# Optimization experiments

Hardware: AMD Instinct MI355X
Metric: run time of the kernel (lower is better)

The kernel has to match this reference:

```python
import jax, jax.numpy as jnp
import numpy as np

DIM = 128  # feature dim, used for 1/sqrt(dim) scaling


def setup_inputs() -> dict:
    key = jax.random.key(0)
    kq, kk, kv, kpq, kpk = jax.random.split(key, 5)
    B, S, D = 16, 2048, DIM
    return {
        "Q": jax.random.normal(kq, (B, S, D), dtype=jnp.float32),
        "K": jax.random.normal(kk, (B, S, D), dtype=jnp.float32),
        "V": jax.random.normal(kv, (B, S, D), dtype=jnp.float32),
        "p_q": jax.random.uniform(kpq, (B, S, 1), dtype=jnp.float32),
        "p_k": jax.random.uniform(kpk, (B, S, 1), dtype=jnp.float32),
    }


def reference(Q, K, V, p_q, p_k):
    # A: [B, Sq, Sk] scaled dot-product scores
    scale = 1.0 / jnp.sqrt(jnp.asarray(DIM, dtype=Q.dtype))
    A = jnp.einsum("bqd,bkd->bqk", Q, K) * scale
    # multiplicative pre-gate: p_q [B,Sq,1] * p_k^T [B,1,Sk]
    A = A * p_q * jnp.swapaxes(p_k, -2, -1)
    W = jax.nn.softmax(A, axis=-1)
    return jnp.einsum("bqk,bkd->bqd", W, V)
```

## Files before the change

kernel.cpp:

```cpp
#include <hip/hip_runtime.h>
#include <hip/hip_fp16.h>


typedef _Float16 f16x8 __attribute__((ext_vector_type(8)));
typedef float f32x16 __attribute__((ext_vector_type(16)));
typedef unsigned int u32x4 __attribute__((ext_vector_type(4)));

#define S_LEN 2048
#define DD 128
#define TILE_BYTES 16384
#define NT 32

#define EXP2(x) __builtin_amdgcn_exp2f(x)

__device__ __forceinline__ unsigned int pk2(float a, float b) {
  __half2 h = __float22half2_rn(make_float2(a, b));
  return __builtin_bit_cast(unsigned int, h);
}

__device__ __forceinline__ void st8(void* dst, const float v[8]) {
  u32x4 u;
  u[0] = pk2(v[0], v[1]);
  u[1] = pk2(v[2], v[3]);
  u[2] = pk2(v[4], v[5]);
  u[3] = pk2(v[6], v[7]);
  *(u32x4*)dst = u;
}

__device__ __forceinline__ void gld16(const void* g, void* l) {
  __builtin_amdgcn_global_load_lds(
      (const __attribute__((address_space(1))) unsigned int*)g,
      (__attribute__((address_space(3))) unsigned int*)l, 16, 0, 0);
}

__global__ __launch_bounds__(256) void prep_q_k(const float* __restrict__ Q,
                                                const float* __restrict__ pq,
                                                char* __restrict__ qh) {
  size_t i = ((size_t)blockIdx.x * 256 + threadIdx.x) * 8;
  const float g = pq[i >> 7] * 0.12751743343158394f;
  float4 a = *(const float4*)(Q + i);
  float4 b = *(const float4*)(Q + i + 4);
  float v[8] = {a.x * g, a.y * g, a.z * g, a.w * g,
                b.x * g, b.y * g, b.z * g, b.w * g};
  st8(qh + i * 2, v);
}

__global__ __launch_bounds__(256) void prep_kv(
    const float* __restrict__ K, const float* __restrict__ V,
    const float* __restrict__ pk, char* __restrict__ kimg,
    char* __restrict__ vimg) {
  __shared__ float vt[64 * 132];
  const int t = threadIdx.x;
  const int bid = blockIdx.x;
  const int bq = bid & 15;
  const int kt = bid >> 4;
  const size_t rowbase = (size_t)bq * S_LEN + kt * 64;

#pragma unroll
  for (int cc = 0; cc < 8; ++cc) {
    const int f = cc * 256 + t;
    const int row = f >> 5;
    const int col = (f & 31) * 4;
    *(float4*)(vt + row * 132 + col) = *(const float4*)(V + (rowbase + row) * DD + col);
  }

  char* kdst = kimg + (size_t)(bq * NT + kt) * TILE_BYTES;
#pragma unroll
  for (int cc = 0; cc < 4; ++cc) {
    const int p0 = (cc * 256 + t) * 16;
    const int key = p0 >> 8;
    const int d0 = ((p0 & 255) ^ ((key & 7) << 4)) >> 1;
    const float g = pk[rowbase + key];
    const float* src = K + (rowbase + key) * DD + d0;
    float4 a = *(const float4*)(src);
    float4 b = *(const float4*)(src + 4);
    float v[8] = {a.x * g, a.y * g, a.z * g, a.w * g,
                  b.x * g, b.y * g, b.z * g, b.w * g};
    st8(kdst + p0, v);
  }

  __syncthreads();

  char* vdst = vimg + (size_t)(bq * NT + kt) * TILE_BYTES;
#pragma unroll
  for (int cc = 0; cc < 4; ++cc) {
    const int p0 = (cc * 256 + t) * 16;
    const int dcol = p0 >> 7;
    const int key0 = ((p0 & 127) ^ ((dcol & 7) << 4)) >> 1;
    float v[8];
#pragma unroll
    for (int j = 0; j < 8; ++j) v[j] = vt[(key0 + j) * 132 + dcol];
    st8(vdst + p0, v);
  }
}

__global__ __launch_bounds__(512, 2) void attn_main(const char* __restrict__ qh,
                                                    const char* __restrict__ kimg,
                                                    const char* __restrict__ vimg,
                                                    float* __restrict__ out) {
  __shared__ float4 ldsraw[4352];
  char* lds = (char*)ldsraw;
  const int tid = threadIdx.x;
  const int wid = tid >> 6;
  const int qs = wid >> 1;
  const int ks = wid & 1;
  const int lane = tid & 63;
  const int c = lane & 31;
  const int h = lane >> 5;
  const int swz = (c & 7) << 4;
  const int bid = blockIdx.x;
  const int bq = 2 * (bid & 7) + ((bid >> 3) & 1);
  const int qt = bid >> 4;
  const int q0 = qt * 128 + qs * 32;

  f16x8 qf[8];
  const char* qrow = qh + (size_t)(bq * S_LEN + q0 + c) * (DD * 2);
#pragma unroll
  for (int kc = 0; kc < 8; ++kc) qf[kc] = *(const f16x8*)(qrow + kc * 32 + h * 16);

  f32x16 acc[4];
#pragma unroll
  for (int d = 0; d < 4; ++d) {
#pragma unroll
    for (int r = 0; r < 16; ++r) acc[d][r] = 0.f;
  }
  float m_run = -1.0e30f, l_run = 0.f;

  const char* kb = kimg + (size_t)bq * (NT * TILE_BYTES);
  const char* vb = vimg + (size_t)bq * (NT * TILE_BYTES);

#pragma unroll
  for (int j = 0; j < 2; ++j) {
    gld16(kb + j * 8192 + tid * 16, lds + j * 8192 + tid * 16);
    gld16(vb + j * 8192 + tid * 16, lds + TILE_BYTES + j * 8192 + tid * 16);
  }

  for (int kt = 0; kt < NT; ++kt) {
    __syncthreads();
    const int cur = (kt & 1) << 15;
    if (kt + 1 < NT) {
      const int nxt = ((kt + 1) & 1) << 15;
      const char* kn = kb + (size_t)(kt + 1) * TILE_BYTES;
      const char* vn = vb + (size_t)(kt + 1) * TILE_BYTES;
#pragma unroll
      for (int j = 0; j < 2; ++j) {
        gld16(kn + j * 8192 + tid * 16, lds + nxt + j * 8192 + tid * 16);
        gld16(vn + j * 8192 + tid * 16, lds + nxt + TILE_BYTES + j * 8192 + tid * 16);
      }
    }
    const char* kl = lds + cur;
    const char* vl = lds + cur + TILE_BYTES;

    f32x16 s;
#pragma unroll
    for (int r = 0; r < 16; ++r) s[r] = 0.f;
    __builtin_amdgcn_s_setprio(1);
#pragma unroll
    for (int kc = 0; kc < 8; ++kc) {
      f16x8 kf = *(const f16x8*)(kl + (ks * 32 + c) * 256 + ((kc * 32 + h * 16) ^ swz));
      s = __builtin_amdgcn_mfma_f32_32x32x16_f16(kf, qf[kc], s, 0, 0, 0);
    }
    __builtin_amdgcn_s_setprio(0);

    float cm = s[0];
#pragma unroll
    for (int r = 1; r < 16; ++r) cm = fmaxf(cm, s[r]);
    cm = fmaxf(cm, __shfl_xor(cm, 32));
    if (__any(cm > m_run + 11.0f)) {
      const float mn = fmaxf(m_run, cm);
      const float al = EXP2(m_run - mn);
      m_run = mn;
      l_run *= al;
#pragma unroll
      for (int d = 0; d < 4; ++d) {
#pragma unroll
        for (int r = 0; r < 16; ++r) acc[d][r] *= al;
      }
    }
    float ps = 0.f;
#pragma unroll
    for (int r = 0; r < 16; ++r) {
      s[r] = EXP2(s[r] - m_run);
      ps += s[r];
    }
    l_run += ps;

#pragma unroll
    for (int kc = 0; kc < 2; ++kc) {
      const int A = kc * 8;
      const int Bb = A + 4;
      unsigned pA0 = pk2(s[A + 0], s[A + 1]);
      unsigned pA1 = pk2(s[A + 2], s[A + 3]);
      unsigned pB0 = pk2(s[Bb + 0], s[Bb + 1]);
      unsigned pB1 = pk2(s[Bb + 2], s[Bb + 3]);
      unsigned own0 = h ? pB0 : pA0;
      unsigned own1 = h ? pB1 : pA1;
      unsigned snd0 = h ? pA0 : pB0;
      unsigned snd1 = h ? pA1 : pB1;
      unsigned rcv0 = __shfl_xor(snd0, 32);
      unsigned rcv1 = __shfl_xor(snd1, 32);
      u32x4 pw;
      pw[0] = h ? rcv0 : own0;
      pw[1] = h ? rcv1 : own1;
      pw[2] = h ? own0 : rcv0;
      pw[3] = h ? own1 : rcv1;
      f16x8 pf = __builtin_bit_cast(f16x8, pw);
      const int kci = ks * 2 + kc;
      __builtin_amdgcn_s_setprio(1);
#pragma unroll
      for (int d = 0; d < 4; ++d) {
        f16x8 vf = *(const f16x8*)(vl + (d * 32 + c) * 128 + ((kci * 32 + h * 16) ^ swz));
        acc[d] = __builtin_amdgcn_mfma_f32_32x32x16_f16(vf, pf, acc[d], 0, 0, 0);
      }
      __builtin_amdgcn_s_setprio(0);
    }
  }

  l_run += __shfl_xor(l_run, 32);

  __syncthreads();
  float2* ml = (float2*)(lds + 65536);
  if (h == 0) ml[wid * 32 + c] = make_float2(m_run, l_run);
  __syncthreads();
  const float2 po = ml[(wid ^ 1) * 32 + c];
  const float ms = fmaxf(m_run, po.x);
  const float lstar = l_run * EXP2(m_run - ms) + po.y * EXP2(po.x - ms);
  const float w = EXP2(m_run - ms) / lstar;

  char* T = lds;
  if (ks == 0) {
#pragma unroll
    for (int d = 0; d < 4; ++d) {
#pragma unroll
      for (int rr = 0; rr < 4; ++rr) {
        const int dd = d * 32 + rr * 8 + h * 4;
        float4 v4;
        v4.x = acc[d][rr * 4 + 0] * w;
        v4.y = acc[d][rr * 4 + 1] * w;
        v4.z = acc[d][rr * 4 + 2] * w;
        v4.w = acc[d][rr * 4 + 3] * w;
        *(float4*)(T + (qs * 32 + c) * 512 + ((dd * 4) ^ swz)) = v4;
      }
    }
  }
  __syncthreads();
  if (ks == 1) {
#pragma unroll
    for (int d = 0; d < 4; ++d) {
#pragma unroll
      for (int rr = 0; rr < 4; ++rr) {
        const int dd = d * 32 + rr * 8 + h * 4;
        float4* p = (float4*)(T + (qs * 32 + c) * 512 + ((dd * 4) ^ swz));
        float4 t = *p;
        t.x += acc[d][rr * 4 + 0] * w;
        t.y += acc[d][rr * 4 + 1] * w;
        t.z += acc[d][rr * 4 + 2] * w;
        t.w += acc[d][rr * 4 + 3] * w;
        *p = t;
      }
    }
  }
  __syncthreads();

  float* obase = out + ((size_t)bq * S_LEN + qt * 128) * DD;
#pragma unroll
  for (int p = 0; p < 8; ++p) {
    const int idx = p * 512 + tid;
    const int q = idx >> 5;
    const int d0 = (idx & 31) * 4;
    float4 v4 = *(const float4*)(T + q * 512 + ((d0 * 4) ^ ((q & 7) << 4)));
    *(float4*)(obase + q * DD + d0) = v4;
  }
}

extern "C" void kernel_launch(void* const* d_in, const int* in_sizes, int n_in,
                              void* d_out, int out_size, void* d_ws, size_t ws_size,
                              hipStream_t stream) {
  const float* Q = (const float*)d_in[0];
  const float* K = (const float*)d_in[1];
  const float* V = (const float*)d_in[2];
  const float* pq = (const float*)d_in[3];
  const float* pk = (const float*)d_in[4];
  float* out = (float*)d_out;
  char* ws = (char*)d_ws;
  char* qh = ws;
  char* kimg = ws + (8u << 20);
  char* vimg = ws + (16u << 20);

  prep_q_k<<<2048, 256, 0, stream>>>(Q, pq, qh);
  prep_kv<<<512, 256, 0, stream>>>(K, V, pk, kimg, vimg);
  attn_main<<<256, 512, 0, stream>>>(qh, kimg, vimg, out);
}
```

Before: 66.33 us.

## Split attention over two key halves and merge partials in separate kernel

Splits the key/value sequence into two halves so attn_main launches 512 blocks instead of 256, each processing 16 key tiles. Every block writes an fp16 partial output plus its running max and sum, and a new merge2 kernel combines the two halves with softmax rescaling into the fp32 output. This targets low occupancy on a GPU with many CUs (256 blocks underfill it), at the cost of an extra launch, extra global traffic for the partials, and fp16 rounding of intermediate outputs. It also tree-reduces the max and splits the exp-sum into two accumulators to shorten dependency chains, and changes launch bounds to 4 blocks per SM with a smaller LDS array.

```diff
diff --git a/kernel.cpp b/kernel.cpp
--- a/kernel.cpp
+++ b/kernel.cpp
@@ -10,6 +10,9 @@
 #define DD 128
 #define TILE_BYTES 16384
 #define NT 32
+#define NTH 16
+#define PART_ROWS 32768
+#define PART_STRIDE 4194304
 
 #define EXP2(x) __builtin_amdgcn_exp2f(x)
 
@@ -94,11 +97,12 @@
   }
 }
 
-__global__ __launch_bounds__(512, 2) void attn_main(const char* __restrict__ qh,
+__global__ __launch_bounds__(512, 4) void attn_main(const char* __restrict__ qh,
                                                     const char* __restrict__ kimg,
                                                     const char* __restrict__ vimg,
-                                                    float* __restrict__ out) {
-  __shared__ float4 ldsraw[4352];
+                                                    _Float16* __restrict__ part,
+                                                    float2* __restrict__ mlws) {
+  __shared__ float4 ldsraw[4224];
   char* lds = (char*)ldsraw;
   const int tid = threadIdx.x;
   const int wid = tid >> 6;
@@ -110,7 +114,8 @@
   const int swz = (c & 7) << 4;
   const int bid = blockIdx.x;
   const int bq = 2 * (bid & 7) + ((bid >> 3) & 1);
-  const int qt = bid >> 4;
+  const int qt = (bid >> 4) & 15;
+  const int kh = bid >> 8;
   const int q0 = qt * 128 + qs * 32;
 
   f16x8 qf[8];
@@ -126,8 +131,8 @@
   }
   float m_run = -1.0e30f, l_run = 0.f;
 
-  const char* kb = kimg + (size_t)bq * (NT * TILE_BYTES);
-  const char* vb = vimg + (size_t)bq * (NT * TILE_BYTES);
+  const char* kb = kimg + (size_t)(bq * NT + kh * NTH) * TILE_BYTES;
+  const char* vb = vimg + (size_t)(bq * NT + kh * NTH) * TILE_BYTES;
 
 #pragma unroll
   for (int j = 0; j < 2; ++j) {
@@ -135,10 +140,10 @@
     gld16(vb + j * 8192 + tid * 16, lds + TILE_BYTES + j * 8192 + tid * 16);
   }
 
-  for (int kt = 0; kt < NT; ++kt) {
+  for (int kt = 0; kt < NTH; ++kt) {
     __syncthreads();
     const int cur = (kt & 1) << 15;
-    if (kt + 1 < NT) {
+    if (kt + 1 < NTH) {
       const int nxt = ((kt + 1) & 1) << 15;
       const char* kn = kb + (size_t)(kt + 1) * TILE_BYTES;
       const char* vn = vb + (size_t)(kt + 1) * TILE_BYTES;
@@ -162,9 +167,12 @@
     }
     __builtin_amdgcn_s_setprio(0);
 
-    float cm = s[0];
-#pragma unroll
-    for (int r = 1; r < 16; ++r) cm = fmaxf(cm, s[r]);
+    float m0 = fmaxf(s[0], s[1]), m1 = fmaxf(s[2], s[3]);
+    float m2 = fmaxf(s[4], s[5]), m3 = fmaxf(s[6], s[7]);
+    float m4 = fmaxf(s[8], s[9]), m5 = fmaxf(s[10], s[11]);
+    float m6 = fmaxf(s[12], s[13]), m7 = fmaxf(s[14], s[15]);
+    m0 = fmaxf(m0, m1); m2 = fmaxf(m2, m3); m4 = fmaxf(m4, m5); m6 = fmaxf(m6, m7);
+    float cm = fmaxf(fmaxf(m0, m2), fmaxf(m4, m6));
     cm = fmaxf(cm, __shfl_xor(cm, 32));
     if (__any(cm > m_run + 11.0f)) {
       const float mn = fmaxf(m_run, cm);
@@ -177,13 +185,13 @@
         for (int r = 0; r < 16; ++r) acc[d][r] *= al;
       }
     }
-    float ps = 0.f;
-#pragma unroll
-    for (int r = 0; r < 16; ++r) {
-      s[r] = EXP2(s[r] - m_run);
-      ps += s[r];
-    }
-    l_run += ps;
+    float ps0 = 0.f, ps1 = 0.f;
+#pragma unroll
+    for (int r = 0; r < 8; ++r) {
+      s[r] = EXP2(s[r] - m_run);         ps0 += s[r];
+      s[r + 8] = EXP2(s[r + 8] - m_run); ps1 += s[r + 8];
+    }
+    l_run += ps0 + ps1;
 
 #pragma unroll
     for (int kc = 0; kc < 2; ++kc) {
@@ -262,15 +270,50 @@
   }
   __syncthreads();
 
-  float* obase = out + ((size_t)bq * S_LEN + qt * 128) * DD;
-#pragma unroll
-  for (int p = 0; p < 8; ++p) {
+  const size_t prow = (size_t)bq * S_LEN + qt * 128;
+  _Float16* pdst = part + (size_t)kh * PART_STRIDE + prow * 128;
+#pragma unroll
+  for (int p = 0; p < 4; ++p) {
     const int idx = p * 512 + tid;
-    const int q = idx >> 5;
-    const int d0 = (idx & 31) * 4;
-    float4 v4 = *(const float4*)(T + q * 512 + ((d0 * 4) ^ ((q & 7) << 4)));
-    *(float4*)(obase + q * DD + d0) = v4;
-  }
+    const int row = idx >> 4;
+    const int d0 = (idx & 15) * 8;
+    const int swzT = (row & 7) << 4;
+    float4 A = *(const float4*)(T + row * 512 + ((d0 * 4) ^ swzT));
+    float4 Bv = *(const float4*)(T + row * 512 + (((d0 * 4) + 16) ^ swzT));
+    float v[8] = {A.x, A.y, A.z, A.w, Bv.x, Bv.y, Bv.z, Bv.w};
+    st8((void*)(pdst + row * 128 + d0), v);
+  }
+  if (ks == 0 && h == 0)
+    mlws[(size_t)kh * PART_ROWS + prow + qs * 32 + c] = make_float2(ms, lstar);
+}
+
+__global__ __launch_bounds__(256) void merge2(const _Float16* __restrict__ part,
+                                              const float2* __restrict__ mlws,
+                                              float* __restrict__ out) {
+  const int t = blockIdx.x * 256 + threadIdx.x;
+  const int d0 = (t & 15) * 8;
+  const int r = t >> 4;
+  const float2 a = mlws[r];
+  const float2 b = mlws[PART_ROWS + r];
+  const float M = fmaxf(a.x, b.x);
+  const float wa = a.y * EXP2(a.x - M);
+  const float wb = b.y * EXP2(b.x - M);
+  const float inv = 1.f / (wa + wb);
+  const float fa = wa * inv, fb = wb * inv;
+  const f16x8 pa = *(const f16x8*)(part + (size_t)r * 128 + d0);
+  const f16x8 pb = *(const f16x8*)(part + PART_STRIDE + (size_t)r * 128 + d0);
+  float4 o0, o1;
+  o0.x = fa * (float)pa[0] + fb * (float)pb[0];
+  o0.y = fa * (float)pa[1] + fb * (float)pb[1];
+  o0.z = fa * (float)pa[2] + fb * (float)pb[2];
+  o0.w = fa * (float)pa[3] + fb * (float)pb[3];
+  o1.x = fa * (float)pa[4] + fb * (float)pb[4];
+  o1.y = fa * (float)pa[5] + fb * (float)pb[5];
+  o1.z = fa * (float)pa[6] + fb * (float)pb[6];
+  o1.w = fa * (float)pa[7] + fb * (float)pb[7];
+  float* orow = out + (size_t)r * 128 + d0;
+  *(float4*)orow = o0;
+  *(float4*)(orow + 4) = o1;
 }
 
 extern "C" void kernel_launch(void* const* d_in, const int* in_sizes, int n_in,
@@ -286,8 +329,11 @@
   char* qh = ws;
   char* kimg = ws + (8u << 20);
   char* vimg = ws + (16u << 20);
+  _Float16* part = (_Float16*)(ws + (24u << 20));
+  float2* mlws = (float2*)(ws + (42u << 20));
 
   prep_q_k<<<2048, 256, 0, stream>>>(Q, pq, qh);
   prep_kv<<<512, 256, 0, stream>>>(K, V, pk, kimg, vimg);
-  attn_main<<<256, 512, 0, stream>>>(qh, kimg, vimg, out);
-}
+  attn_main<<<512, 512, 0, stream>>>(qh, kimg, vimg, part, mlws);
+  merge2<<<2048, 256, 0, stream>>>(part, mlws, out);
+}
```

After: 149.7 us. 2.26x slower.

## Software-pipeline QK^T one tile ahead with triple-buffered K in LDS

Applied to the files above, without the earlier changes.

Restructures the main loop so the QK^T MFMA for tile kt+1 is issued before the softmax and PV of tile kt, so score math for the next tile can overlap the exp/pack work of the current one. K moves to a triple buffer loaded two tiles ahead, V stays double-buffered, and LDS grows to 80KB. The max and sum reductions are also split into trees to shorten dependency chains. The cost is more registers (two score accumulators) and more LDS, which may reduce occupancy at 2 blocks per CU.

```diff
diff --git a/kernel.cpp b/kernel.cpp
--- a/kernel.cpp
+++ b/kernel.cpp
@@ -12,6 +12,9 @@
 #define NT 32
 
 #define EXP2(x) __builtin_amdgcn_exp2f(x)
+
+#define LDS_VBASE 49152
+#define LDS_ML 65536
 
 __device__ __forceinline__ unsigned int pk2(float a, float b) {
   __half2 h = __float22half2_rn(make_float2(a, b));
@@ -98,7 +101,7 @@
                                                     const char* __restrict__ kimg,
                                                     const char* __restrict__ vimg,
                                                     float* __restrict__ out) {
-  __shared__ float4 ldsraw[4352];
+  __shared__ float4 ldsraw[5120];
   char* lds = (char*)ldsraw;
   const int tid = threadIdx.x;
   const int wid = tid >> 6;
@@ -132,39 +135,64 @@
 #pragma unroll
   for (int j = 0; j < 2; ++j) {
     gld16(kb + j * 8192 + tid * 16, lds + j * 8192 + tid * 16);
-    gld16(vb + j * 8192 + tid * 16, lds + TILE_BYTES + j * 8192 + tid * 16);
-  }
-
+    gld16(kb + TILE_BYTES + j * 8192 + tid * 16, lds + TILE_BYTES + j * 8192 + tid * 16);
+    gld16(vb + j * 8192 + tid * 16, lds + LDS_VBASE + j * 8192 + tid * 16);
+  }
+  __syncthreads();
+
+  const int krow_off = (ks * 32 + c) * 256;
+  f32x16 sA;
+#pragma unroll
+  for (int r = 0; r < 16; ++r) sA[r] = 0.f;
+  __builtin_amdgcn_s_setprio(1);
+#pragma unroll
+  for (int kc = 0; kc < 8; ++kc) {
+    f16x8 kf = *(const f16x8*)(lds + krow_off + ((kc * 32 + h * 16) ^ swz));
+    sA = __builtin_amdgcn_mfma_f32_32x32x16_f16(kf, qf[kc], sA, 0, 0, 0);
+  }
+  __builtin_amdgcn_s_setprio(0);
+
+  int kwr = 2;
+  int krd = 1;
+#pragma unroll 2
   for (int kt = 0; kt < NT; ++kt) {
     __syncthreads();
-    const int cur = (kt & 1) << 15;
+
+    if (kt + 2 < NT) {
+      const char* kn = kb + (size_t)(kt + 2) * TILE_BYTES;
+      char* kdst = lds + kwr * TILE_BYTES;
+#pragma unroll
+      for (int j = 0; j < 2; ++j)
+        gld16(kn + j * 8192 + tid * 16, kdst + j * 8192 + tid * 16);
+    }
     if (kt + 1 < NT) {
-      const int nxt = ((kt + 1) & 1) << 15;
-      const char* kn = kb + (size_t)(kt + 1) * TILE_BYTES;
       const char* vn = vb + (size_t)(kt + 1) * TILE_BYTES;
-#pragma unroll
-      for (int j = 0; j < 2; ++j) {
-        gld16(kn + j * 8192 + tid * 16, lds + nxt + j * 8192 + tid * 16);
-        gld16(vn + j * 8192 + tid * 16, lds + nxt + TILE_BYTES + j * 8192 + tid * 16);
-      }
-    }
-    const char* kl = lds + cur;
-    const char* vl = lds + cur + TILE_BYTES;
-
-    f32x16 s;
-#pragma unroll
-    for (int r = 0; r < 16; ++r) s[r] = 0.f;
-    __builtin_amdgcn_s_setprio(1);
-#pragma unroll
-    for (int kc = 0; kc < 8; ++kc) {
-      f16x8 kf = *(const f16x8*)(kl + (ks * 32 + c) * 256 + ((kc * 32 + h * 16) ^ swz));
-      s = __builtin_amdgcn_mfma_f32_32x32x16_f16(kf, qf[kc], s, 0, 0, 0);
-    }
-    __builtin_amdgcn_s_setprio(0);
-
-    float cm = s[0];
-#pragma unroll
-    for (int r = 1; r < 16; ++r) cm = fmaxf(cm, s[r]);
+      char* vdst = lds + LDS_VBASE + ((kt + 1) & 1) * TILE_BYTES;
+#pragma unroll
+      for (int j = 0; j < 2; ++j)
+        gld16(vn + j * 8192 + tid * 16, vdst + j * 8192 + tid * 16);
+    }
+
+    f32x16 sB;
+#pragma unroll
+    for (int r = 0; r < 16; ++r) sB[r] = 0.f;
+    if (kt + 1 < NT) {
+      const char* kl = lds + krd * TILE_BYTES;
+      __builtin_amdgcn_s_setprio(1);
+#pragma unroll
+      for (int kc = 0; kc < 8; ++kc) {
+        f16x8 kf = *(const f16x8*)(kl + krow_off + ((kc * 32 + h * 16) ^ swz));
+        sB = __builtin_amdgcn_mfma_f32_32x32x16_f16(kf, qf[kc], sB, 0, 0, 0);
+      }
+      __builtin_amdgcn_s_setprio(0);
+    }
+
+    float m0 = fmaxf(sA[0], sA[1]), m1 = fmaxf(sA[2], sA[3]);
+    float m2 = fmaxf(sA[4], sA[5]), m3 = fmaxf(sA[6], sA[7]);
+    float m4 = fmaxf(sA[8], sA[9]), m5 = fmaxf(sA[10], sA[11]);
+    float m6 = fmaxf(sA[12], sA[13]), m7 = fmaxf(sA[14], sA[15]);
+    m0 = fmaxf(m0, m1); m2 = fmaxf(m2, m3); m4 = fmaxf(m4, m5); m6 = fmaxf(m6, m7);
+    float cm = fmaxf(fmaxf(m0, m2), fmaxf(m4, m6));
     cm = fmaxf(cm, __shfl_xor(cm, 32));
     if (__any(cm > m_run + 11.0f)) {
       const float mn = fmaxf(m_run, cm);
@@ -177,22 +205,23 @@
         for (int r = 0; r < 16; ++r) acc[d][r] *= al;
       }
     }
-    float ps = 0.f;
-#pragma unroll
-    for (int r = 0; r < 16; ++r) {
-      s[r] = EXP2(s[r] - m_run);
-      ps += s[r];
-    }
-    l_run += ps;
-
+    float ps0 = 0.f, ps1 = 0.f;
+#pragma unroll
+    for (int r = 0; r < 8; ++r) {
+      sA[r] = EXP2(sA[r] - m_run);         ps0 += sA[r];
+      sA[r + 8] = EXP2(sA[r + 8] - m_run); ps1 += sA[r + 8];
+    }
+    l_run += ps0 + ps1;
+
+    const char* vl = lds + LDS_VBASE + (kt & 1) * TILE_BYTES;
 #pragma unroll
     for (int kc = 0; kc < 2; ++kc) {
       const int A = kc * 8;
       const int Bb = A + 4;
-      unsigned pA0 = pk2(s[A + 0], s[A + 1]);
-      unsigned pA1 = pk2(s[A + 2], s[A + 3]);
-      unsigned pB0 = pk2(s[Bb + 0], s[Bb + 1]);
-      unsigned pB1 = pk2(s[Bb + 2], s[Bb + 3]);
+      unsigned pA0 = pk2(sA[A + 0], sA[A + 1]);
+      unsigned pA1 = pk2(sA[A + 2], sA[A + 3]);
+      unsigned pB0 = pk2(sA[Bb + 0], sA[Bb + 1]);
+      unsigned pB1 = pk2(sA[Bb + 2], sA[Bb + 3]);
       unsigned own0 = h ? pB0 : pA0;
       unsigned own1 = h ? pB1 : pA1;
       unsigned snd0 = h ? pA0 : pB0;
@@ -214,12 +243,16 @@
       }
       __builtin_amdgcn_s_setprio(0);
     }
+
+    sA = sB;
+    krd = (krd == 2) ? 0 : krd + 1;
+    kwr = (kwr == 2) ? 0 : kwr + 1;
   }
 
   l_run += __shfl_xor(l_run, 32);
 
   __syncthreads();
-  float2* ml = (float2*)(lds + 65536);
+  float2* ml = (float2*)(lds + LDS_ML);
   if (h == 0) ml[wid * 32 + c] = make_float2(m_run, l_run);
   __syncthreads();
   const float2 po = ml[(wid ^ 1) * 32 + c];
```

Result: no change. 66.67 us (+0.5%).
